# Optimization experiments

Measured on AMD Instinct MI355X. Metric: run time of the kernel, lower is better.

The kernel has to match this reference:

```python
import jax, jax.numpy as jnp
import numpy as np

L, H, NH, NKV, HD, S, P, FF = 2, 2048, 16, 2, 128, 1024, 1024, 5632
G = NH // NKV
THETA = 1000000.0
EPS = 1e-6
SCALE = 1.0 / np.sqrt(HD).astype(np.float32)


def rms_norm(x, w):
    return x * jax.lax.rsqrt(jnp.mean(x * x, axis=-1, keepdims=True) + EPS) * w


def rotate_half(x):
    x1, x2 = jnp.split(x, 2, axis=-1)
    return jnp.concatenate([-x2, x1], axis=-1)


def setup_inputs() -> dict:
    key = jax.random.key(0)
    ks = iter(jax.random.split(key, 16))
    w = lambda shape: jax.random.normal(next(ks), shape, jnp.float32) * 0.02
    return {
        'inputs_embeds': jax.random.normal(next(ks), (1, S, H), jnp.float32),
        'position_ids': (jnp.arange(S, dtype=jnp.int32) + P)[None, :],
        'past_k': jax.random.normal(next(ks), (L, 1, NKV, P, HD), jnp.float32),
        'past_v': jax.random.normal(next(ks), (L, 1, NKV, P, HD), jnp.float32),
        'ln1_w': jnp.ones((L, H), jnp.float32),
        'wq': w((L, H, NH * HD)), 'bq': jnp.zeros((L, NH * HD), jnp.float32),
        'wk': w((L, H, NKV * HD)), 'bk': jnp.zeros((L, NKV * HD), jnp.float32),
        'wv': w((L, H, NKV * HD)), 'bv': jnp.zeros((L, NKV * HD), jnp.float32),
        'wo': w((L, NH * HD, H)),
        'ln2_w': jnp.ones((L, H), jnp.float32),
        'w_gate': w((L, H, FF)), 'w_up': w((L, H, FF)), 'w_down': w((L, FF, H)),
        'norm_w': jnp.ones((H,), jnp.float32),
    }


def reference(inputs_embeds, position_ids, past_k, past_v, ln1_w, wq, bq, wk, bk,
              wv, bv, wo, ln2_w, w_gate, w_up, w_down, norm_w):
    pos = position_ids.astype(jnp.float32)                      # [1,S]
    inv_freq = 1.0 / (THETA ** (jnp.arange(0, HD, 2, dtype=jnp.float32) / HD))
    freqs = pos[:, :, None] * inv_freq                          # [1,S,HD/2]
    emb = jnp.concatenate([freqs, freqs], axis=-1)              # [1,S,HD]
    cos = jnp.cos(emb)[:, None]                                 # [1,1,S,HD]
    sin = jnp.sin(emb)[:, None]
    T = P + S
    k_pos = jnp.arange(T, dtype=jnp.float32)
    # causal mask over absolute positions: future keys masked with -65504
    mask = jnp.where(k_pos[None, None, None, :] > pos[:, None, :, None],
                     jnp.float32(-65504.0), jnp.float32(0.0))   # [1,1,S,T]

    hidden = inputs_embeds
    present = []
    for i in range(L):
        residual = hidden
        h = rms_norm(hidden, ln1_w[i])
        q = (h @ wq[i] + bq[i]).reshape(1, S, NH, HD).transpose(0, 2, 1, 3)
        k = (h @ wk[i] + bk[i]).reshape(1, S, NKV, HD).transpose(0, 2, 1, 3)
        v = (h @ wv[i] + bv[i]).reshape(1, S, NKV, HD).transpose(0, 2, 1, 3)
        q = q * cos + rotate_half(q) * sin
        k = k * cos + rotate_half(k) * sin
        k = jnp.concatenate([past_k[i], k], axis=2)             # [1,NKV,T,HD]
        v = jnp.concatenate([past_v[i], v], axis=2)
        present.append(k)
        present.append(v)
        # GQA: group query heads per kv head instead of expanding k/v
        qg = q.reshape(1, NKV, G, S, HD)
        attn = jnp.einsum('bkgsd,bktd->bkgst', qg, k) * SCALE   # [1,NKV,G,S,T]
        attn = jax.nn.softmax(attn + mask[:, :, None], axis=-1)
        out = jnp.einsum('bkgst,bktd->bkgsd', attn, v)
        out = out.reshape(1, NH, S, HD).transpose(0, 2, 1, 3).reshape(1, S, H)
        hidden = residual + out @ wo[i]
        residual = hidden
        h = rms_norm(hidden, ln2_w[i])
        h = (jax.nn.silu(h @ w_gate[i]) * (h @ w_up[i])) @ w_down[i]
        hidden = residual + h
    hidden = rms_norm(hidden, norm_w)
    return (hidden, *present)
```

## Files before the change

### kernel.cpp

```cpp
#include <hip/hip_runtime.h>

#define L_ 2
#define H_ 2048
#define NH_ 16
#define NKV_ 2
#define HD_ 128
#define S_ 1024
#define P_ 1024
#define T_ 2048
#define FF_ 5632
#define QKVN_ 2560
#define KOFF_ 2048
#define VOFF_ 2304

#define EPS_ 1e-6f
#define SCALE_ 0.08838834764831845f
#define DEFER_THR_ 8.0f

typedef __bf16 bf16_t;
typedef unsigned int u32;
typedef __bf16 bx8 __attribute__((ext_vector_type(8)));
typedef __bf16 bx4 __attribute__((ext_vector_type(4)));
typedef float  fx4 __attribute__((ext_vector_type(4)));

__device__ __forceinline__ fx4 mfma16(bx8 a, bx8 b, fx4 c) {
  return __builtin_amdgcn_mfma_f32_16x16x32_bf16(a, b, c, 0, 0, 0);
}

#define GLL16(gsrc, ldst) __builtin_amdgcn_global_load_lds( \
    (__attribute__((address_space(1))) void*)(gsrc),        \
    (__attribute__((address_space(3))) void*)(ldst), 16, 0, 0)

__device__ __forceinline__ bx8 lds_read_b128(char* p) {
  u32 a = (u32)(uintptr_t)(__attribute__((address_space(3))) void*)p;
  bx8 d;
  asm volatile("ds_read_b128 %0, %1" : "=v"(d) : "v"(a));
  return d;
}
__device__ __forceinline__ void lds_write_b16(char* p, float v) {
  u32 a = (u32)(uintptr_t)(__attribute__((address_space(3))) void*)p;
  bf16_t b = (bf16_t)v;
  u32 d = (u32)__builtin_bit_cast(unsigned short, b);
  asm volatile("ds_write_b16 %0, %1" :: "v"(a), "v"(d));
}

#define LGKM(n) asm volatile("s_waitcnt lgkmcnt(" #n ")" ::: "memory"); __builtin_amdgcn_sched_barrier(0)

__device__ __forceinline__ int xcd_swizzle(int orig, int nwg) {
  int q = nwg >> 3, r = nwg & 7;
  int xcd = orig & 7, lid = orig >> 3;
  return (xcd < r ? xcd * (q + 1) : r * (q + 1) + (xcd - r) * q) + lid;
}

__global__ void k_rope_tables(const int* __restrict__ pos, float* __restrict__ ct, float* __restrict__ st) {
  int i = blockIdx.x * 256 + threadIdx.x;
  if (i >= S_ * 64) return;
  int s = i >> 6, d = i & 63;
  float p = (float)pos[s];
  float inv = expf(-(float)(2 * d) * (13.815510557964274f / 128.0f));
  float f = p * inv;
  ct[i] = cosf(f);
  st[i] = sinf(f);
}

__global__ void k_copy4(const float* __restrict__ in, float* __restrict__ out, int n4) {
  int i = blockIdx.x * 256 + threadIdx.x;
  if (i < n4) ((fx4*)out)[i] = ((const fx4*)in)[i];
}

__global__ void k_cbias(const float* __restrict__ bq, const float* __restrict__ bk,
                        const float* __restrict__ bv, float* __restrict__ cb) {
  int i = blockIdx.x * 256 + threadIdx.x;
  if (i >= L_ * QKVN_) return;
  int l = i / QKVN_, j = i % QKVN_;
  float v;
  if (j < KOFF_)      v = bq[l * KOFF_ + j];
  else if (j < VOFF_) v = bk[l * (NKV_ * HD_) + j - KOFF_];
  else                v = bv[l * (NKV_ * HD_) + j - VOFF_];
  cb[i] = v;
}

template<int OUTBF>
__global__ __launch_bounds__(256) void k_rmsnorm(const float* __restrict__ x, const float* __restrict__ w,
                                                 void* __restrict__ y) {
  int row = blockIdx.x, tid = threadIdx.x;
  const fx4* xr = (const fx4*)(x + (size_t)row * H_);
  fx4 v0 = xr[tid], v1 = xr[tid + 256];
  float ss = v0[0]*v0[0] + v0[1]*v0[1] + v0[2]*v0[2] + v0[3]*v0[3]
           + v1[0]*v1[0] + v1[1]*v1[1] + v1[2]*v1[2] + v1[3]*v1[3];
  #pragma unroll
  for (int off = 32; off > 0; off >>= 1) ss += __shfl_xor(ss, off);
  __shared__ float red[4];
  if ((tid & 63) == 0) red[tid >> 6] = ss;
  __syncthreads();
  float tot = red[0] + red[1] + red[2] + red[3];
  float rs = rsqrtf(tot * (1.0f / H_) + EPS_);
  const fx4* wr_ = (const fx4*)w;
  fx4 w0 = wr_[tid], w1 = wr_[tid + 256];
  if (OUTBF) {
    bf16_t* yb = (bf16_t*)y + (size_t)row * H_;
    bx4 o0, o1;
    #pragma unroll
    for (int i = 0; i < 4; i++) { o0[i] = (bf16_t)(v0[i] * rs * w0[i]); o1[i] = (bf16_t)(v1[i] * rs * w1[i]); }
    *(bx4*)&yb[tid * 4] = o0;
    *(bx4*)&yb[(tid + 256) * 4] = o1;
  } else {
    float* yf = (float*)y + (size_t)row * H_;
    fx4 o0, o1;
    #pragma unroll
    for (int i = 0; i < 4; i++) { o0[i] = v0[i] * rs * w0[i]; o1[i] = v1[i] * rs * w1[i]; }
    *(fx4*)&yf[tid * 4] = o0;
    *(fx4*)&yf[(tid + 256) * 4] = o1;
  }
}

__global__ __launch_bounds__(256) void k_transpose_w(const float* __restrict__ in, bf16_t* __restrict__ out,
                                                     int R, int C) {
  __shared__ __attribute__((aligned(16))) float Tt[64 * 68];
  int tid = threadIdx.x;
  int c0 = blockIdx.x * 64, r0 = blockIdx.y * 64;
  #pragma unroll
  for (int j = 0; j < 4; j++) {
    int c = j * 256 + tid;
    int row = c >> 4, col = (c & 15) * 4;
    *(fx4*)&Tt[row * 68 + col] = *(const fx4*)&in[(size_t)(r0 + row) * C + c0 + col];
  }
  __syncthreads();
  #pragma unroll
  for (int j = 0; j < 2; j++) {
    int c = j * 256 + tid;
    int n = c >> 3, ko = (c & 7) * 8;
    bx8 o;
    #pragma unroll
    for (int i = 0; i < 8; i++) o[i] = (bf16_t)Tt[(ko + i) * 68 + n];
    *(bx8*)&out[(size_t)(c0 + n) * R + r0 + ko] = o;
  }
}

template<int OUTBF, int HASB, int HASR, int HASG, int SPLIT>
__global__ __launch_bounds__(256) void k_gemm(const bf16_t* __restrict__ A, const bf16_t* __restrict__ Bt,
                                              const float* __restrict__ bias, const float* __restrict__ res,
                                              const bf16_t* __restrict__ gmul,
                                              void* __restrict__ out, int M, int N, int lda, int kLen, int gy) {
  __shared__ __attribute__((aligned(16))) bf16_t sA[2][64 * 64];
  __shared__ __attribute__((aligned(16))) bf16_t sB[2][128 * 64];
  int tid = threadIdx.x;
  int w = tid >> 6, lane = tid & 63, g = lane >> 4, r = lane & 15;
  int wr = w >> 1, wc = w & 1;
  int swzid = xcd_swizzle((int)blockIdx.x, (int)gridDim.x);
  int per = (int)gridDim.x / SPLIT;
  int sp = swzid / per;
  int rem = swzid - sp * per;
  int m0 = (rem % gy) * 64;
  int n0 = (rem / gy) * 128;
  A  += (size_t)sp * kLen;
  Bt += (size_t)sp * kLen;
  fx4 acc[2][4] = {};
  int swz = (r & 7) << 4;
  int col0 = (g * 16) ^ swz;
  int col1 = (64 + g * 16) ^ swz;
  int wbase = (tid & ~63) * 16;
  int nk = kLen >> 6;

  auto STAGE = [&](int buf, int k0) {
    #pragma unroll
    for (int j = 0; j < 2; j++) {
      int d = (j * 256 + tid) * 16;
      int row = d >> 7;
      int inrow = (d & 127) ^ ((row & 7) << 4);
      GLL16((const char*)(A + (size_t)(m0 + row) * lda + k0) + inrow,
            (char*)&sA[buf][0] + j * 4096 + wbase);
    }
    #pragma unroll
    for (int j = 0; j < 4; j++) {
      int d = (j * 256 + tid) * 16;
      int row = d >> 7;
      int inrow = (d & 127) ^ ((row & 7) << 4);
      GLL16((const char*)(Bt + (size_t)(n0 + row) * lda + k0) + inrow,
            (char*)&sB[buf][0] + j * 4096 + wbase);
    }
  };

  STAGE(0, 0);
  int cur = 0;
  for (int t = 0; t < nk; t++) {
    if (t + 1 < nk) {
      STAGE(cur ^ 1, (t + 1) << 6);
      asm volatile("s_waitcnt vmcnt(6)" ::: "memory");
    } else {
      asm volatile("s_waitcnt vmcnt(0)" ::: "memory");
    }
    __builtin_amdgcn_s_barrier();
    __builtin_amdgcn_sched_barrier(0);
    char* pa = (char*)&sA[cur][0] + (wr * 32 + r) * 128;
    char* pb = (char*)&sB[cur][0] + (wc * 64 + r) * 128;
    bx8 fa[2][2], fb[4][2];
    fa[0][0] = lds_read_b128(pa + col0);
    fa[1][0] = lds_read_b128(pa + 2048 + col0);
    #pragma unroll
    for (int n = 0; n < 4; n++) fb[n][0] = lds_read_b128(pb + n * 2048 + col0);
    fa[0][1] = lds_read_b128(pa + col1);
    fa[1][1] = lds_read_b128(pa + 2048 + col1);
    #pragma unroll
    for (int n = 0; n < 4; n++) fb[n][1] = lds_read_b128(pb + n * 2048 + col1);
    LGKM(6);
    __builtin_amdgcn_s_setprio(1);
    #pragma unroll
    for (int n = 0; n < 4; n++) {
      acc[0][n] = mfma16(fa[0][0], fb[n][0], acc[0][n]);
      acc[1][n] = mfma16(fa[1][0], fb[n][0], acc[1][n]);
    }
    __builtin_amdgcn_s_setprio(0);
    LGKM(0);
    __builtin_amdgcn_s_setprio(1);
    #pragma unroll
    for (int n = 0; n < 4; n++) {
      acc[0][n] = mfma16(fa[0][1], fb[n][1], acc[0][n]);
      acc[1][n] = mfma16(fa[1][1], fb[n][1], acc[1][n]);
    }
    __builtin_amdgcn_s_setprio(0);
    if (t + 1 < nk) {
      __builtin_amdgcn_s_barrier();
      __builtin_amdgcn_sched_barrier(0);
    }
    cur ^= 1;
  }
  #pragma unroll
  for (int m = 0; m < 2; m++)
    #pragma unroll
    for (int n = 0; n < 4; n++) {
      int col = n0 + wc * 64 + n * 16 + r;
      #pragma unroll
      for (int rr = 0; rr < 4; rr++) {
        int row = m0 + wr * 32 + m * 16 + 4 * g + rr;
        float v = acc[m][n][rr];
        if (SPLIT > 1) {
          atomicAdd(&((float*)out)[(size_t)row * N + col], v);
        } else {
          if (HASB) v += bias[col];
          if (HASR) v += res[(size_t)row * N + col];
          if (HASG) {
            float x = (float)gmul[(size_t)row * N + col];
            v = (x / (1.0f + __expf(-x))) * v;
          }
          if (OUTBF) ((bf16_t*)out)[(size_t)row * N + col] = (bf16_t)v;
          else       ((float*)out)[(size_t)row * N + col] = v;
        }
      }
    }
}

__global__ void k_rope_q(const bf16_t* __restrict__ qkv, const float* __restrict__ ct,
                         const float* __restrict__ st, bf16_t* __restrict__ qout) {
  int i = blockIdx.x * 256 + threadIdx.x;
  if (i >= S_ * NH_ * 64) return;
  int d = i & 63, h = (i >> 6) & 15, s = i >> 10;
  size_t ib = (size_t)s * QKVN_ + h * HD_;
  float x1 = (float)qkv[ib + d];
  float x2 = (float)qkv[ib + d + 64];
  float c = ct[s * 64 + d], sn = st[s * 64 + d];
  size_t ob = ((size_t)h * S_ + s) * HD_;
  qout[ob + d]      = (bf16_t)(x1 * c - x2 * sn);
  qout[ob + d + 64] = (bf16_t)(x2 * c + x1 * sn);
}

__global__ void k_build_k(const bf16_t* __restrict__ qkv, const float* __restrict__ pastk,
                          const float* __restrict__ ct, const float* __restrict__ st,
                          bf16_t* __restrict__ kc, float* __restrict__ pk_out) {
  int i = blockIdx.x * 256 + threadIdx.x;
  if (i >= NKV_ * T_ * 64) return;
  int d = i & 63, t = (i >> 6) & (T_ - 1), kv = i >> 17;
  size_t cb = ((size_t)kv * T_ + t) * HD_;
  if (t < P_) {
    size_t pb = ((size_t)kv * P_ + t) * HD_;
    float a = pastk[pb + d], b = pastk[pb + d + 64];
    kc[cb + d] = (bf16_t)a; kc[cb + d + 64] = (bf16_t)b;
    pk_out[cb + d] = a;     pk_out[cb + d + 64] = b;
  } else {
    int s = t - P_;
    size_t ib = (size_t)s * QKVN_ + KOFF_ + kv * HD_;
    float x1 = (float)qkv[ib + d];
    float x2 = (float)qkv[ib + d + 64];
    float c = ct[s * 64 + d], sn = st[s * 64 + d];
    float k1 = x1 * c - x2 * sn, k2 = x2 * c + x1 * sn;
    kc[cb + d] = (bf16_t)k1; kc[cb + d + 64] = (bf16_t)k2;
    pk_out[cb + d] = k1;     pk_out[cb + d + 64] = k2;
  }
}

__global__ __launch_bounds__(256) void k_build_vt(const bf16_t* __restrict__ qkv, const float* __restrict__ pastv,
                                                  bf16_t* __restrict__ vt, float* __restrict__ pv_out) {
  int t0 = blockIdx.x * 64, d0 = blockIdx.y * 64, kv = blockIdx.z;
  __shared__ __attribute__((aligned(16))) float Tt[64 * 68];
  int tid = threadIdx.x;
  if (t0 < P_) {
    #pragma unroll
    for (int j = 0; j < 4; j++) {
      int c = j * 256 + tid;
      int row = c >> 4, col = (c & 15) * 4;
      int t = t0 + row;
      fx4 v = *(const fx4*)&pastv[((size_t)kv * P_ + t) * HD_ + d0 + col];
      *(fx4*)&Tt[row * 68 + col] = v;
      *(fx4*)&pv_out[((size_t)kv * T_ + t) * HD_ + d0 + col] = v;
    }
  } else {
    #pragma unroll
    for (int j = 0; j < 4; j++) {
      int c = j * 256 + tid;
      int row = c >> 4, col = (c & 15) * 4;
      int t = t0 + row;
      bx4 b = *(const bx4*)&qkv[(size_t)(t - P_) * QKVN_ + VOFF_ + kv * HD_ + d0 + col];
      fx4 v;
      #pragma unroll
      for (int q = 0; q < 4; q++) v[q] = (float)b[q];
      *(fx4*)&Tt[row * 68 + col] = v;
      *(fx4*)&pv_out[((size_t)kv * T_ + t) * HD_ + d0 + col] = v;
    }
  }
  __syncthreads();
  #pragma unroll
  for (int j = 0; j < 2; j++) {
    int c = j * 256 + tid;
    int n = c >> 3, ko = (c & 7) * 8;
    bx8 o;
    #pragma unroll
    for (int i = 0; i < 8; i++) o[i] = (bf16_t)Tt[(ko + i) * 68 + n];
    *(bx8*)&vt[((size_t)kv * HD_ + d0 + n) * T_ + t0 + ko] = o;
  }
}

__global__ __launch_bounds__(128) void k_attn(const bf16_t* __restrict__ Q, const bf16_t* __restrict__ Kc,
                                              const bf16_t* __restrict__ VT, bf16_t* __restrict__ O) {
  __shared__ __attribute__((aligned(16))) bf16_t Klds[2][64 * 128];
  __shared__ __attribute__((aligned(16))) bf16_t Vlds[2][128 * 64];
  __shared__ __attribute__((aligned(16))) bf16_t Plds[2][16][72];
  int tid = threadIdx.x;
  int w = tid >> 6, lane = tid & 63, g = lane >> 4, r = lane & 15;
  int b = blockIdx.x;
  int half = b >> 8;
  int idx = b & 255;
  int cx = idx & 31;
  int chunk = half ? (31 - cx) : cx;
  int h = (half << 3) | (idx >> 5);
  int kv = half;
  int m0 = chunk * 32;
  int qr0 = m0 + w * 16;
  const bf16_t* qb = Q + ((size_t)h * S_ + qr0 + r) * HD_ + g * 8;
  bx8 qf[4];
  #pragma unroll
  for (int kc = 0; kc < 4; kc++) qf[kc] = *(const bx8*)(qb + kc * 32);
  fx4 of[8] = {};
  float mrun[4], lrun[4];
  #pragma unroll
  for (int i = 0; i < 4; i++) { mrun[i] = -1e30f; lrun[i] = 0.0f; }
  int lim = P_ + qr0 + 4 * g;
  int ntile = (P_ + m0 + 32 + 63) >> 6;
  const char* kg = (const char*)(Kc + (size_t)kv * T_ * HD_);
  const char* vg = (const char*)(VT + (size_t)kv * HD_ * T_);
  int wbase = (tid & ~63) * 16;

  auto STAGE = [&](int buf, int t0) {
    #pragma unroll
    for (int j = 0; j < 8; j++) {
      int D = j * 2048 + tid * 16;
      int row = D >> 8, inrow = D & 255;
      const char* src = kg + (size_t)(t0 + row) * 256 + (inrow ^ ((row & 7) << 4));
      GLL16(src, (char*)&Klds[buf][0] + j * 2048 + wbase);
    }
    #pragma unroll
    for (int j = 0; j < 8; j++) {
      int D = j * 2048 + tid * 16;
      int row = D >> 7, inrow = D & 127;
      const char* src = vg + (size_t)row * 4096 + (size_t)t0 * 2 + (inrow ^ ((row & 7) << 4));
      GLL16(src, (char*)&Vlds[buf][0] + j * 2048 + wbase);
    }
  };

  STAGE(0, 0);
  asm volatile("s_waitcnt vmcnt(0)" ::: "memory");
  __builtin_amdgcn_s_barrier();
  __builtin_amdgcn_sched_barrier(0);
  int cur = 0;
  for (int t = 0; t < ntile; t++) {
    int t0 = t * 64;
    if (t + 1 < ntile) {
      STAGE(cur ^ 1, t0 + 64);
      asm volatile("s_waitcnt vmcnt(16)" ::: "memory");
    } else {
      asm volatile("s_waitcnt vmcnt(0)" ::: "memory");
    }
    __builtin_amdgcn_s_barrier();
    __builtin_amdgcn_sched_barrier(0);
    char* kb = (char*)&Klds[cur][0];
    char* vb = (char*)&Vlds[cur][0];
    bx8 kf[4][4];
    #pragma unroll
    for (int nt = 0; nt < 4; nt++) {
      int row = nt * 16 + r;
      char* kr = kb + row * 256;
      int sz = (row & 7) << 4;
      #pragma unroll
      for (int kc = 0; kc < 4; kc++)
        kf[nt][kc] = lds_read_b128(kr + (((kc * 32 + g * 8) * 2) ^ sz));
    }
    fx4 sc[4] = {};
    LGKM(12);
    #pragma unroll
    for (int kc = 0; kc < 4; kc++) sc[0] = mfma16(qf[kc], kf[0][kc], sc[0]);
    LGKM(8);
    #pragma unroll
    for (int kc = 0; kc < 4; kc++) sc[1] = mfma16(qf[kc], kf[1][kc], sc[1]);
    LGKM(4);
    #pragma unroll
    for (int kc = 0; kc < 4; kc++) sc[2] = mfma16(qf[kc], kf[2][kc], sc[2]);
    LGKM(0);
    #pragma unroll
    for (int kc = 0; kc < 4; kc++) sc[3] = mfma16(qf[kc], kf[3][kc], sc[3]);
    bx8 vf0[8], vf1[8];
    #pragma unroll
    for (int dt = 0; dt < 8; dt++) {
      int row = dt * 16 + r;
      vf0[dt] = lds_read_b128(vb + row * 128 + (((g * 8) * 2) ^ ((row & 7) << 4)));
    }
    #pragma unroll
    for (int dt = 0; dt < 8; dt++) {
      int row = dt * 16 + r;
      vf1[dt] = lds_read_b128(vb + row * 128 + (((32 + g * 8) * 2) ^ ((row & 7) << 4)));
    }
    float lm[4] = {-1e30f, -1e30f, -1e30f, -1e30f};
    #pragma unroll
    for (int nt = 0; nt < 4; nt++)
      #pragma unroll
      for (int rr = 0; rr < 4; rr++) {
        int key = t0 + nt * 16 + r;
        float sv = sc[nt][rr] * SCALE_;
        sv = (key > lim + rr) ? -1e30f : sv;
        sc[nt][rr] = sv;
        lm[rr] = fmaxf(lm[rr], sv);
      }
    int ok = (lm[0] <= mrun[0] + DEFER_THR_) & (lm[1] <= mrun[1] + DEFER_THR_) &
             (lm[2] <= mrun[2] + DEFER_THR_) & (lm[3] <= mrun[3] + DEFER_THR_);
    if (!__all(ok)) {
      float av[4];
      #pragma unroll
      for (int off = 1; off < 16; off <<= 1)
        #pragma unroll
        for (int rr = 0; rr < 4; rr++) lm[rr] = fmaxf(lm[rr], __shfl_xor(lm[rr], off));
      #pragma unroll
      for (int rr = 0; rr < 4; rr++) {
        float mn = fmaxf(mrun[rr], lm[rr]);
        av[rr] = __expf(mrun[rr] - mn);
        mrun[rr] = mn;
        lrun[rr] *= av[rr];
      }
      #pragma unroll
      for (int f = 0; f < 8; f++)
        #pragma unroll
        for (int rr = 0; rr < 4; rr++) of[f][rr] *= av[rr];
    }
    #pragma unroll
    for (int nt = 0; nt < 2; nt++)
      #pragma unroll
      for (int rr = 0; rr < 4; rr++) {
        float pr = __expf(sc[nt][rr] - mrun[rr]);
        lrun[rr] += pr;
        lds_write_b16((char*)&Plds[w][4 * g + rr][nt * 16 + r], pr);
      }
    bx8 pa0 = lds_read_b128((char*)&Plds[w][r][g * 8]);
    #pragma unroll
    for (int nt = 2; nt < 4; nt++)
      #pragma unroll
      for (int rr = 0; rr < 4; rr++) {
        float pr = __expf(sc[nt][rr] - mrun[rr]);
        lrun[rr] += pr;
        lds_write_b16((char*)&Plds[w][4 * g + rr][nt * 16 + r], pr);
      }
    bx8 pa1 = lds_read_b128((char*)&Plds[w][r][32 + g * 8]);
    LGKM(9);
    #pragma unroll
    for (int dt = 0; dt < 8; dt++) of[dt] = mfma16(pa0, vf0[dt], of[dt]);
    LGKM(0);
    #pragma unroll
    for (int dt = 0; dt < 8; dt++) of[dt] = mfma16(pa1, vf1[dt], of[dt]);
    __builtin_amdgcn_s_barrier();
    cur ^= 1;
  }
  #pragma unroll
  for (int off = 1; off < 16; off <<= 1)
    #pragma unroll
    for (int rr = 0; rr < 4; rr++) lrun[rr] += __shfl_xor(lrun[rr], off);
  float li[4];
  #pragma unroll
  for (int rr = 0; rr < 4; rr++) li[rr] = 1.0f / lrun[rr];
  #pragma unroll
  for (int dt = 0; dt < 8; dt++)
    #pragma unroll
    for (int rr = 0; rr < 4; rr++)
      O[(size_t)(qr0 + 4 * g + rr) * H_ + h * HD_ + dt * 16 + r] = (bf16_t)(of[dt][rr] * li[rr]);
}

extern "C" void kernel_launch(void* const* d_in, const int* in_sizes, int n_in,
                              void* d_out, int out_size, void* d_ws, size_t ws_size,
                              hipStream_t stream) {
  const float* embeds = (const float*)d_in[0];
  const int*   pos    = (const int*)d_in[1];
  const float* past_k = (const float*)d_in[2];
  const float* past_v = (const float*)d_in[3];
  const float* ln1    = (const float*)d_in[4];
  const float* wq     = (const float*)d_in[5];
  const float* bq     = (const float*)d_in[6];
  const float* wk     = (const float*)d_in[7];
  const float* bk     = (const float*)d_in[8];
  const float* wv     = (const float*)d_in[9];
  const float* bv     = (const float*)d_in[10];
  const float* wo     = (const float*)d_in[11];
  const float* ln2    = (const float*)d_in[12];
  const float* wg     = (const float*)d_in[13];
  const float* wu     = (const float*)d_in[14];
  const float* wd     = (const float*)d_in[15];
  const float* normw  = (const float*)d_in[16];

  char* wsp = (char*)d_ws;
  auto take = [&](size_t n) { char* p = wsp; wsp += (n + 255) & ~(size_t)255; return (void*)p; };
  float*  cos_t  = (float*)take((size_t)S_ * 64 * 4);
  float*  sin_t  = (float*)take((size_t)S_ * 64 * 4);
  float*  cbias  = (float*)take((size_t)L_ * QKVN_ * 4);
  float*  hidden = (float*)take((size_t)S_ * H_ * 4);
  bf16_t* hnorm  = (bf16_t*)take((size_t)S_ * H_ * 2);
  bf16_t* qkv    = (bf16_t*)take((size_t)S_ * QKVN_ * 2);
  bf16_t* qrope  = (bf16_t*)take((size_t)NH_ * S_ * HD_ * 2);
  bf16_t* kcache = (bf16_t*)take((size_t)NKV_ * T_ * HD_ * 2);
  bf16_t* vtr    = (bf16_t*)take((size_t)NKV_ * HD_ * T_ * 2);
  bf16_t* attno  = (bf16_t*)take((size_t)S_ * H_ * 2);
  bf16_t* gateb  = (bf16_t*)take((size_t)S_ * FF_ * 2);
  bf16_t* hgb    = (bf16_t*)take((size_t)S_ * FF_ * 2);
  bf16_t* wT     = (bf16_t*)take((size_t)FF_ * H_ * 2);

  float* out_h = (float*)d_out;

  k_rope_tables<<<256, 256, 0, stream>>>(pos, cos_t, sin_t);
  k_cbias<<<(L_ * QKVN_ + 255) / 256, 256, 0, stream>>>(bq, bk, bv, cbias);
  k_copy4<<<(S_ * H_ / 4 + 255) / 256, 256, 0, stream>>>(embeds, hidden, S_ * H_ / 4);

  for (int l = 0; l < L_; l++) {
    const float* wq_l = wq + (size_t)l * H_ * (NH_ * HD_);
    const float* wk_l = wk + (size_t)l * H_ * (NKV_ * HD_);
    const float* wv_l = wv + (size_t)l * H_ * (NKV_ * HD_);
    const float* wo_l = wo + (size_t)l * (NH_ * HD_) * H_;
    const float* wg_l = wg + (size_t)l * H_ * FF_;
    const float* wu_l = wu + (size_t)l * H_ * FF_;
    const float* wd_l = wd + (size_t)l * FF_ * H_;
    const float* pk_in = past_k + (size_t)l * NKV_ * P_ * HD_;
    const float* pv_in = past_v + (size_t)l * NKV_ * P_ * HD_;
    float* pk_out = out_h + (size_t)S_ * H_ + (size_t)l * 2 * NKV_ * T_ * HD_;
    float* pv_out = pk_out + (size_t)NKV_ * T_ * HD_;

    k_rmsnorm<1><<<S_, 256, 0, stream>>>(hidden, ln1 + (size_t)l * H_, hnorm);
    k_transpose_w<<<dim3(32, 32), 256, 0, stream>>>(wq_l, wT, H_, NH_ * HD_);
    k_transpose_w<<<dim3(4, 32), 256, 0, stream>>>(wk_l, wT + (size_t)KOFF_ * H_, H_, NKV_ * HD_);
    k_transpose_w<<<dim3(4, 32), 256, 0, stream>>>(wv_l, wT + (size_t)VOFF_ * H_, H_, NKV_ * HD_);
    k_gemm<1, 1, 0, 0, 1><<<(QKVN_ / 128) * (S_ / 64), 256, 0, stream>>>(
        hnorm, wT, cbias + (size_t)l * QKVN_, nullptr, nullptr, qkv, S_, QKVN_, H_, H_, S_ / 64);
    k_rope_q<<<(S_ * NH_ * 64) / 256, 256, 0, stream>>>(qkv, cos_t, sin_t, qrope);
    k_build_k<<<(NKV_ * T_ * 64) / 256, 256, 0, stream>>>(qkv, pk_in, cos_t, sin_t, kcache, pk_out);
    k_build_vt<<<dim3(T_ / 64, HD_ / 64, NKV_), 256, 0, stream>>>(qkv, pv_in, vtr, pv_out);
    k_attn<<<512, 128, 0, stream>>>(qrope, kcache, vtr, attno);
    k_transpose_w<<<dim3(32, 32), 256, 0, stream>>>(wo_l, wT, NH_ * HD_, H_);
    k_gemm<0, 0, 1, 0, 1><<<(H_ / 128) * (S_ / 64), 256, 0, stream>>>(
        attno, wT, nullptr, hidden, nullptr, hidden, S_, H_, NH_ * HD_, NH_ * HD_, S_ / 64);
    k_rmsnorm<1><<<S_, 256, 0, stream>>>(hidden, ln2 + (size_t)l * H_, hnorm);
    k_transpose_w<<<dim3(88, 32), 256, 0, stream>>>(wg_l, wT, H_, FF_);
    k_gemm<1, 0, 0, 0, 1><<<(FF_ / 128) * (S_ / 64), 256, 0, stream>>>(
        hnorm, wT, nullptr, nullptr, nullptr, gateb, S_, FF_, H_, H_, S_ / 64);
    k_transpose_w<<<dim3(88, 32), 256, 0, stream>>>(wu_l, wT, H_, FF_);
    k_gemm<1, 0, 0, 1, 1><<<(FF_ / 128) * (S_ / 64), 256, 0, stream>>>(
        hnorm, wT, nullptr, nullptr, gateb, hgb, S_, FF_, H_, H_, S_ / 64);
    k_transpose_w<<<dim3(32, 88), 256, 0, stream>>>(wd_l, wT, FF_, H_);
    k_gemm<0, 0, 0, 0, 2><<<2 * (H_ / 128) * (S_ / 64), 256, 0, stream>>>(
        hgb, wT, nullptr, nullptr, nullptr, hidden, S_, H_, FF_, FF_ / 2, S_ / 64);
  }
  k_rmsnorm<0><<<S_, 256, 0, stream>>>(hidden, normw, out_h);
}
```

Baseline: 556.4 us.

## Add 128x128 double-buffered GEMM for MLP and split-K the output projection

Adds a new GEMM kernel with 128x128 output tiles per block, a 4x4 MFMA fragment grid per wave and a double-buffered LDS pipeline. The gate, up and down MLP projections now use it. The larger tile raises data reuse per byte loaded and halves the block count. The output projection switches to split-K of 2 with atomic accumulation into the residual hidden buffer. This doubles its block count but relies on atomics and on hidden already holding the residual. The bigger tiles use more registers and LDS per block, which may lower occupancy, and MLP grids drop to 352 and 256 blocks.

```diff
diff --git a/kernel.cpp b/kernel.cpp
--- a/kernel.cpp
+++ b/kernel.cpp
@@ -250,6 +250,116 @@
     }
 }
 
+template<int OUTBF, int HASG, int SPLIT>
+__global__ __launch_bounds__(256) void k_gemm_big(const bf16_t* __restrict__ A, const bf16_t* __restrict__ Bt,
+                                                  const bf16_t* __restrict__ gmul,
+                                                  void* __restrict__ out, int M, int N, int lda, int kLen, int gy) {
+  __shared__ __attribute__((aligned(16))) bf16_t sA[2][128 * 64];
+  __shared__ __attribute__((aligned(16))) bf16_t sB[2][128 * 64];
+  int tid = threadIdx.x;
+  int w = tid >> 6, lane = tid & 63, g = lane >> 4, r = lane & 15;
+  int wr = w >> 1, wc = w & 1;
+  int swzid = xcd_swizzle((int)blockIdx.x, (int)gridDim.x);
+  int per = (int)gridDim.x / SPLIT;
+  int sp = swzid / per;
+  int rem = swzid - sp * per;
+  int m0 = (rem % gy) * 128;
+  int n0 = (rem / gy) * 128;
+  A  += (size_t)sp * kLen;
+  Bt += (size_t)sp * kLen;
+  fx4 acc[4][4] = {};
+  int swz = (r & 7) << 4;
+  int col0 = (g * 16) ^ swz;
+  int col1 = (64 + g * 16) ^ swz;
+  int wbase = (tid & ~63) * 16;
+  int nk = kLen >> 6;
+
+  auto STAGE = [&](int buf, int k0) {
+    #pragma unroll
+    for (int j = 0; j < 4; j++) {
+      int d = (j * 256 + tid) * 16;
+      int row = d >> 7;
+      int inrow = (d & 127) ^ ((row & 7) << 4);
+      GLL16((const char*)(A + (size_t)(m0 + row) * lda + k0) + inrow,
+            (char*)&sA[buf][0] + j * 4096 + wbase);
+    }
+    #pragma unroll
+    for (int j = 0; j < 4; j++) {
+      int d = (j * 256 + tid) * 16;
+      int row = d >> 7;
+      int inrow = (d & 127) ^ ((row & 7) << 4);
+      GLL16((const char*)(Bt + (size_t)(n0 + row) * lda + k0) + inrow,
+            (char*)&sB[buf][0] + j * 4096 + wbase);
+    }
+  };
+
+  STAGE(0, 0);
+  int cur = 0;
+  for (int t = 0; t < nk; t++) {
+    if (t + 1 < nk) {
+      STAGE(cur ^ 1, (t + 1) << 6);
+      asm volatile("s_waitcnt vmcnt(8)" ::: "memory");
+    } else {
+      asm volatile("s_waitcnt vmcnt(0)" ::: "memory");
+    }
+    __builtin_amdgcn_s_barrier();
+    __builtin_amdgcn_sched_barrier(0);
+    char* pa = (char*)&sA[cur][0] + (wr * 64 + r) * 128;
+    char* pb = (char*)&sB[cur][0] + (wc * 64 + r) * 128;
+    bx8 fa[4][2], fb[4][2];
+    #pragma unroll
+    for (int m = 0; m < 4; m++) fa[m][0] = lds_read_b128(pa + m * 2048 + col0);
+    #pragma unroll
+    for (int n = 0; n < 4; n++) fb[n][0] = lds_read_b128(pb + n * 2048 + col0);
+    #pragma unroll
+    for (int m = 0; m < 4; m++) fa[m][1] = lds_read_b128(pa + m * 2048 + col1);
+    #pragma unroll
+    for (int n = 0; n < 4; n++) fb[n][1] = lds_read_b128(pb + n * 2048 + col1);
+    LGKM(8);
+    __builtin_amdgcn_s_setprio(1);
+    #pragma unroll
+    for (int m = 0; m < 4; m++)
+      #pragma unroll
+      for (int n = 0; n < 4; n++)
+        acc[m][n] = mfma16(fa[m][0], fb[n][0], acc[m][n]);
+    __builtin_amdgcn_s_setprio(0);
+    LGKM(0);
+    __builtin_amdgcn_s_setprio(1);
+    #pragma unroll
+    for (int m = 0; m < 4; m++)
+      #pragma unroll
+      for (int n = 0; n < 4; n++)
+        acc[m][n] = mfma16(fa[m][1], fb[n][1], acc[m][n]);
+    __builtin_amdgcn_s_setprio(0);
+    if (t + 1 < nk) {
+      __builtin_amdgcn_s_barrier();
+      __builtin_amdgcn_sched_barrier(0);
+    }
+    cur ^= 1;
+  }
+  #pragma unroll
+  for (int m = 0; m < 4; m++)
+    #pragma unroll
+    for (int n = 0; n < 4; n++) {
+      int col = n0 + wc * 64 + n * 16 + r;
+      #pragma unroll
+      for (int rr = 0; rr < 4; rr++) {
+        int row = m0 + wr * 64 + m * 16 + 4 * g + rr;
+        float v = acc[m][n][rr];
+        if (SPLIT > 1) {
+          atomicAdd(&((float*)out)[(size_t)row * N + col], v);
+        } else {
+          if (HASG) {
+            float x = (float)gmul[(size_t)row * N + col];
+            v = (x / (1.0f + __expf(-x))) * v;
+          }
+          if (OUTBF) ((bf16_t*)out)[(size_t)row * N + col] = (bf16_t)v;
+          else       ((float*)out)[(size_t)row * N + col] = v;
+        }
+      }
+    }
+}
+
 __global__ void k_rope_q(const bf16_t* __restrict__ qkv, const float* __restrict__ ct,
                          const float* __restrict__ st, bf16_t* __restrict__ qout) {
   int i = blockIdx.x * 256 + threadIdx.x;
@@ -566,18 +676,18 @@
     k_build_vt<<<dim3(T_ / 64, HD_ / 64, NKV_), 256, 0, stream>>>(qkv, pv_in, vtr, pv_out);
     k_attn<<<512, 128, 0, stream>>>(qrope, kcache, vtr, attno);
     k_transpose_w<<<dim3(32, 32), 256, 0, stream>>>(wo_l, wT, NH_ * HD_, H_);
-    k_gemm<0, 0, 1, 0, 1><<<(H_ / 128) * (S_ / 64), 256, 0, stream>>>(
-        attno, wT, nullptr, hidden, nullptr, hidden, S_, H_, NH_ * HD_, NH_ * HD_, S_ / 64);
+    k_gemm<0, 0, 0, 0, 2><<<2 * (H_ / 128) * (S_ / 64), 256, 0, stream>>>(
+        attno, wT, nullptr, nullptr, nullptr, hidden, S_, H_, NH_ * HD_, (NH_ * HD_) / 2, S_ / 64);
     k_rmsnorm<1><<<S_, 256, 0, stream>>>(hidden, ln2 + (size_t)l * H_, hnorm);
     k_transpose_w<<<dim3(88, 32), 256, 0, stream>>>(wg_l, wT, H_, FF_);
-    k_gemm<1, 0, 0, 0, 1><<<(FF_ / 128) * (S_ / 64), 256, 0, stream>>>(
-        hnorm, wT, nullptr, nullptr, nullptr, gateb, S_, FF_, H_, H_, S_ / 64);
+    k_gemm_big<1, 0, 1><<<(FF_ / 128) * (S_ / 128), 256, 0, stream>>>(
+        hnorm, wT, nullptr, gateb, S_, FF_, H_, H_, S_ / 128);
     k_transpose_w<<<dim3(88, 32), 256, 0, stream>>>(wu_l, wT, H_, FF_);
-    k_gemm<1, 0, 0, 1, 1><<<(FF_ / 128) * (S_ / 64), 256, 0, stream>>>(
-        hnorm, wT, nullptr, nullptr, gateb, hgb, S_, FF_, H_, H_, S_ / 64);
+    k_gemm_big<1, 1, 1><<<(FF_ / 128) * (S_ / 128), 256, 0, stream>>>(
+        hnorm, wT, gateb, hgb, S_, FF_, H_, H_, S_ / 128);
     k_transpose_w<<<dim3(32, 88), 256, 0, stream>>>(wd_l, wT, FF_, H_);
-    k_gemm<0, 0, 0, 0, 2><<<2 * (H_ / 128) * (S_ / 64), 256, 0, stream>>>(
-        hgb, wT, nullptr, nullptr, nullptr, hidden, S_, H_, FF_, FF_ / 2, S_ / 64);
+    k_gemm_big<0, 0, 2><<<2 * (H_ / 128) * (S_ / 128), 256, 0, stream>>>(
+        hgb, wT, nullptr, hidden, S_, H_, FF_, FF_ / 2, S_ / 128);
   }
   k_rmsnorm<0><<<S_, 256, 0, stream>>>(hidden, normw, out_h);
 }
```

After: 558.8 us. About the same (+0.4%).
